# Kernel tuning notes

Hardware: AMD Instinct MI355X
Metric: run time of the kernel (lower is better)

Reference implementation:

```python
import jax, jax.numpy as jnp
import numpy as np

TEMPERATURE = 8.0  # sqrt(d_k=64)
NEG = -1e15


def setup_inputs() -> dict:
    key = jax.random.key(0)
    k1, k2, k3, k4, k5 = jax.random.split(key, 5)
    BH, L, D = 64, 1024, 64  # B=4 examples x H=16 heads
    B = 4
    q = jax.random.normal(k1, (BH, L, D), dtype=jnp.float32)
    k = jax.random.normal(k2, (BH, L, D), dtype=jnp.float32)
    v = jax.random.normal(k3, (BH, L, D), dtype=jnp.float32)
    mask = jax.random.randint(k4, (BH, L, L), 0, 2).astype(jnp.bool_)
    edge = jax.random.randint(k5, (B, L, L), 0, 2).astype(jnp.int32)
    return {"q": q, "k": k, "v": v, "mask": mask, "edge": edge}


def reference(q, k, v, mask, edge):
    # attn = q @ k^T / temperature : [BH, L, L]
    attn = jnp.einsum('bld,bmd->blm', q, k) / TEMPERATURE
    # edge.repeat(BH // B, 1, 1): torch repeat == tile along batch dim
    rep = attn.shape[0] // edge.shape[0]
    edge_t = jnp.tile(edge, (rep, 1, 1))
    attn = jnp.where(edge_t == 0, NEG, attn)
    attn = jnp.where(mask, NEG, attn)
    attn = jax.nn.softmax(attn, axis=2)
    # dropout p=0 -> identity
    output = jnp.einsum('blm,bmd->bld', attn, v)
    return (output, attn)
```

## Files before the change

### kernel.cpp

```cpp
#include <hip/hip_runtime.h>
#include <hip/hip_bf16.h>

#define L_ 1024
#define BH_ 64
#define NEGV (-1e15f)
#define QSCALE 0.18033688011112043f

typedef float f32x4 __attribute__((ext_vector_type(4)));
typedef short s16x8 __attribute__((ext_vector_type(8)));
typedef unsigned short ushort_t;

__device__ __forceinline__ unsigned short f2bf(float f) {
    return __builtin_bit_cast(unsigned short, __float2bfloat16(f));
}
__device__ __forceinline__ unsigned selw(uint4 v, int i) {
    switch (i) { case 0: return v.x; case 1: return v.y; case 2: return v.z; default: return v.w; }
}
__device__ __forceinline__ unsigned spread4(unsigned n) {
    return (n & 1u) | ((n & 2u) << 3) | ((n & 4u) << 6) | ((n & 8u) << 9);
}
__device__ __forceinline__ unsigned pack_bytes_nz(uint4 m) {
    unsigned u = 0;
    #pragma unroll
    for (int k = 0; k < 4; ++k) {
        const unsigned x = selw(m, k);
        u |= ((x & 0x000000FFu) ? 1u : 0u) << (k * 4 + 0);
        u |= ((x & 0x0000FF00u) ? 1u : 0u) << (k * 4 + 1);
        u |= ((x & 0x00FF0000u) ? 1u : 0u) << (k * 4 + 2);
        u |= ((x & 0xFF000000u) ? 1u : 0u) << (k * 4 + 3);
    }
    return u;
}
__device__ __forceinline__ void gl_lds16(const void* g, void* l) {
    __builtin_amdgcn_global_load_lds(
        (const __attribute__((address_space(1))) unsigned int*)g,
        (__attribute__((address_space(3))) unsigned int*)l, 16, 0, 0);
}

template<bool TESTZERO>
__device__ __forceinline__ unsigned row_bits_i32(uint4 e0, uint4 e1, uint4 e2, uint4 e3, int ln)
{
    #define BAL_(v) (TESTZERO ? __ballot((v) == 0u) : __ballot((v) != 0u))
    const unsigned long long b00 = BAL_(e0.x), b01 = BAL_(e0.y), b02 = BAL_(e0.z), b03 = BAL_(e0.w);
    const unsigned long long b10 = BAL_(e1.x), b11 = BAL_(e1.y), b12 = BAL_(e1.z), b13 = BAL_(e1.w);
    const unsigned long long b20 = BAL_(e2.x), b21 = BAL_(e2.y), b22 = BAL_(e2.z), b23 = BAL_(e2.w);
    const unsigned long long b30 = BAL_(e3.x), b31 = BAL_(e3.y), b32 = BAL_(e3.z), b33 = BAL_(e3.w);
    #undef BAL_
    const int q0 = ln >> 4, sh = (ln & 15) << 2;
    unsigned u = 0;
    unsigned long long bp;
    bp = q0 == 0 ? b00 : q0 == 1 ? b10 : q0 == 2 ? b20 : b30;
    u |= spread4((unsigned)((bp >> sh) & 0xF)) << 0;
    bp = q0 == 0 ? b01 : q0 == 1 ? b11 : q0 == 2 ? b21 : b31;
    u |= spread4((unsigned)((bp >> sh) & 0xF)) << 1;
    bp = q0 == 0 ? b02 : q0 == 1 ? b12 : q0 == 2 ? b22 : b32;
    u |= spread4((unsigned)((bp >> sh) & 0xF)) << 2;
    bp = q0 == 0 ? b03 : q0 == 1 ? b13 : q0 == 2 ? b23 : b33;
    u |= spread4((unsigned)((bp >> sh) & 0xF)) << 3;
    return u;
}

__global__ __launch_bounds__(256)
void prep(const float* __restrict__ qp, const float* __restrict__ kp,
          const float* __restrict__ vp, const unsigned char* __restrict__ maskp,
          const int* __restrict__ edgep, ushort_t* __restrict__ ws)
{
    __shared__ float tile[128][68];
    ushort_t* Kp = ws;
    ushort_t* Vp = ws + (1u << 22);
    ushort_t* Qp = ws + (2u << 22);
    ushort_t* Mp = ws + (3u << 22);

    const int b = blockIdx.x;
    const int t = threadIdx.x;

    if (b < 1024) {
        const int wv = t >> 6, ln = t & 63;
        const int rid = (b << 2) + wv;
        const int eb = rid >> 10, row = rid & 1023;

        unsigned det = 0;
        const unsigned* mu = (const unsigned*)maskp;
        #pragma unroll
        for (int i = 0; i < 16; ++i) det |= mu[i];
        const bool mask_i32 = ((det & 0xFFFFFF00u) == 0u);

        unsigned ewv;
        {
            const int rb = ((eb << 10) + row) << 10;
            const uint4 e0 = *((const uint4*)(edgep + rb) + ln);
            const uint4 e1 = *((const uint4*)(edgep + rb + 256) + ln);
            const uint4 e2 = *((const uint4*)(edgep + rb + 512) + ln);
            const uint4 e3 = *((const uint4*)(edgep + rb + 768) + ln);
            ewv = row_bits_i32<true>(e0, e1, e2, e3, ln);
        }
        const int pp = ((ln & 7) << 3) + (ln >> 3);
        for (int bq = 0; bq < 16; ++bq) {
            const int bh = (bq << 2) + eb;
            unsigned u = ewv;
            if (!mask_i32) {
                const uint4 m = *((const uint4*)(maskp + ((size_t)((bh << 10) + row) << 10)) + ln);
                u |= pack_bytes_nz(m);
            } else {
                const int* mp = (const int*)maskp + ((size_t)((bh << 10) + row) << 10);
                const uint4 m0 = *((const uint4*)mp + ln);
                const uint4 m1 = *((const uint4*)(mp + 256) + ln);
                const uint4 m2 = *((const uint4*)(mp + 512) + ln);
                const uint4 m3 = *((const uint4*)(mp + 768) + ln);
                u |= row_bits_i32<false>(m0, m1, m2, m3, ln);
            }
            Mp[((size_t)((bh << 10) + row) << 6) + pp] = (ushort_t)u;
        }
    } else if (b < 1536) {
        const int idx = b - 1024;
        const int bh = idx >> 3, vt = idx & 7;
        const float* vsrc = vp + (((size_t)(bh << 10) + (vt << 7)) << 6);
        #pragma unroll
        for (int i = 0; i < 8; ++i) {
            const int f4 = (i << 8) + t;
            const int k = f4 >> 4, d4 = f4 & 15;
            *(float4*)&tile[k][d4 << 2] = *((const float4*)vsrc + f4);
        }
        __syncthreads();
        ushort_t* dst = Vp + ((size_t)((bh << 3) + vt) << 13);
        #pragma unroll
        for (int i = 0; i < 4; ++i) {
            const int ci = (t << 2) + i;
            const int d = ci >> 4, p = ci & 15;
            const int c = p ^ (d & 7);
            s16x8 o;
            #pragma unroll
            for (int j = 0; j < 8; ++j) o[j] = (short)f2bf(tile[(c << 3) + j][d]);
            *(s16x8*)(dst + (ci << 3)) = o;
        }
    } else if (b < 2048) {
        const int idx = b - 1536;
        const int bh = idx >> 3, kt = idx & 7;
        const int r = t >> 1, h = t & 1;
        const float* src = kp + (((size_t)((bh << 10) + (kt << 7) + r)) << 6) + (h << 5);
        float v[32];
        #pragma unroll
        for (int j = 0; j < 8; ++j) *(float4*)&v[j << 2] = *((const float4*)src + j);
        ushort_t* dst = Kp + ((size_t)((bh << 3) + kt) << 13) + (r << 6);
        #pragma unroll
        for (int q = 0; q < 4; ++q) {
            const int c = (h << 2) + q;
            const int s = c ^ (r & 7);
            s16x8 o;
            #pragma unroll
            for (int j = 0; j < 8; ++j) o[j] = (short)f2bf(v[(q << 3) + j]);
            *(s16x8*)(dst + (s << 3)) = o;
        }
    } else {
        const int bh = b - 2048;
        const int wv = t >> 6, ln = t & 63;
        for (int i = 0; i < 16; ++i) {
            const int rt = (i << 2) + wv;
            const int r = (rt << 4) + (ln & 15), gq = ln >> 4;
            const float* src = qp + (((size_t)((bh << 10) + r)) << 6) + (gq << 3);
            const float4 q0 = *(const float4*)src;
            const float4 q1 = *(const float4*)(src + 4);
            const float4 q2 = *(const float4*)(src + 32);
            const float4 q3 = *(const float4*)(src + 36);
            s16x8 a, bfr;
            a[0]=(short)f2bf(q0.x*QSCALE); a[1]=(short)f2bf(q0.y*QSCALE);
            a[2]=(short)f2bf(q0.z*QSCALE); a[3]=(short)f2bf(q0.w*QSCALE);
            a[4]=(short)f2bf(q1.x*QSCALE); a[5]=(short)f2bf(q1.y*QSCALE);
            a[6]=(short)f2bf(q1.z*QSCALE); a[7]=(short)f2bf(q1.w*QSCALE);
            bfr[0]=(short)f2bf(q2.x*QSCALE); bfr[1]=(short)f2bf(q2.y*QSCALE);
            bfr[2]=(short)f2bf(q2.z*QSCALE); bfr[3]=(short)f2bf(q2.w*QSCALE);
            bfr[4]=(short)f2bf(q3.x*QSCALE); bfr[5]=(short)f2bf(q3.y*QSCALE);
            bfr[6]=(short)f2bf(q3.z*QSCALE); bfr[7]=(short)f2bf(q3.w*QSCALE);
            ushort_t* dst = Qp + ((size_t)((bh << 6) + rt) << 10) + (ln << 4);
            *(s16x8*)(dst) = a;
            *(s16x8*)(dst + 8) = bfr;
        }
    }
}

__global__ __launch_bounds__(512, 4)
void attn_main(const ushort_t* __restrict__ ws, float* __restrict__ outO,
               float* __restrict__ outA)
{
    __shared__ __align__(16) ushort_t p_lds[16 * 1024];
    __shared__ __align__(16) ushort_t stage[2][8192];
    __shared__ float part[16][8];
    __shared__ float gred[16];

    const ushort_t* Kp = ws;
    const ushort_t* Vp = ws + (1u << 22);
    const ushort_t* Qp = ws + (2u << 22);
    const ushort_t* Mp = ws + (3u << 22);

    const int tid = threadIdx.x, lane = tid & 63, w = tid >> 6;
    const int g = lane >> 4, ln = lane & 15;
    const int bid = blockIdx.x, xcd = bid & 7, slot = bid >> 3;
    const int bh = xcd + ((slot >> 6) << 3);
    const int rt = slot & 63;
    const int r0 = rt << 4;
    const int sb = w << 1;

    const ushort_t* qs = Qp + ((size_t)((bh << 6) + rt) << 10) + (lane << 4);
    const s16x8 a0 = *(const s16x8*)(qs);
    const s16x8 a1 = *(const s16x8*)(qs + 8);

    uint4 br[4];
    {
        const ushort_t* mrow = Mp + ((size_t)((bh << 10) + r0 + (g << 2)) << 6) + (w << 3);
        br[0] = *(const uint4*)(mrow);
        br[1] = *(const uint4*)(mrow + 64);
        br[2] = *(const uint4*)(mrow + 128);
        br[3] = *(const uint4*)(mrow + 192);
    }

    #define STAGE_(base, tt, cc)                                                   \
        gl_lds16(base + ((size_t)(bh) << 16) + ((tt) << 13) + ((sb + 0) << 9) + (lane << 3), \
                 &stage[cc][(sb + 0) << 9]);                                       \
        gl_lds16(base + ((size_t)(bh) << 16) + ((tt) << 13) + ((sb + 1) << 9) + (lane << 3), \
                 &stage[cc][(sb + 1) << 9]);

    STAGE_(Kp, 0, 0);
    __syncthreads();

    float rs[4] = {0.f, 0.f, 0.f, 0.f};

    #pragma unroll
    for (int kt = 0; kt < 8; ++kt) {
        const int cur = kt & 1, nxt = cur ^ 1;
        if (kt < 7) { STAGE_(Kp, kt + 1, nxt); }
        else        { STAGE_(Vp, 0, nxt); }

        const int rw = (w << 4) + ln;
        const char* kb = (const char*)stage[cur] + (rw << 7);
        const s16x8 b0 = *(const s16x8*)(kb + (((g)     ^ (rw & 7)) << 4));
        const s16x8 b1 = *(const s16x8*)(kb + (((4 + g) ^ (rw & 7)) << 4));
        f32x4 acc = {0.f, 0.f, 0.f, 0.f};
        acc = __builtin_amdgcn_mfma_f32_16x16x32_bf16(a0, b0, acc, 0, 0, 0);
        acc = __builtin_amdgcn_mfma_f32_16x16x32_bf16(a1, b1, acc, 0, 0, 0);

        #pragma unroll
        for (int reg = 0; reg < 4; ++reg) {
            float sv = acc[reg];
            const unsigned mw = selw(br[reg], kt >> 1);
            if ((mw >> (((kt & 1) << 4) + ln)) & 1u) sv = NEGV;
            const float e = __builtin_amdgcn_exp2f(sv);
            rs[reg] += e;
            const int prow = (g << 2) + reg;
            char* pd = (char*)p_lds + (prow << 11)
                     + ((((kt << 4) + (w << 1) + (ln >> 3)) ^ (prow & 7)) << 4)
                     + ((ln & 7) << 1);
            *(ushort_t*)pd = f2bf(e);
        }
        __syncthreads();
    }

    #pragma unroll
    for (int reg = 0; reg < 4; ++reg) {
        float s = rs[reg];
        s += __shfl_xor(s, 1);
        s += __shfl_xor(s, 2);
        s += __shfl_xor(s, 4);
        s += __shfl_xor(s, 8);
        if (ln == 0) part[(g << 2) + reg][w] = s;
    }
    __syncthreads();
    if (tid < 16) {
        float s = part[tid][0];
        #pragma unroll
        for (int i = 1; i < 8; ++i) s += part[tid][i];
        gred[tid] = __builtin_amdgcn_rcpf(s);
    }
    __syncthreads();

    const int dt = w & 3, kh = w >> 2;
    f32x4 acco = {0.f, 0.f, 0.f, 0.f};
    #pragma unroll
    for (int ut = 0; ut < 8; ++ut) {
        const int cur = ut & 1, nxt = cur ^ 1;
        if (ut < 7) { STAGE_(Vp, ut + 1, nxt); }

        const char* pl = (const char*)p_lds + (ln << 11);
        const s16x8 pa0 = *(const s16x8*)(pl + ((((ut << 4) + (kh << 3) + g)     ^ (ln & 7)) << 4));
        const s16x8 pa1 = *(const s16x8*)(pl + ((((ut << 4) + (kh << 3) + 4 + g) ^ (ln & 7)) << 4));
        const char* vb = (const char*)stage[cur] + (((dt << 4) + ln) << 8);
        const s16x8 vb0 = *(const s16x8*)(vb + ((((kh << 3) + g)     ^ (ln & 7)) << 4));
        const s16x8 vb1 = *(const s16x8*)(vb + ((((kh << 3) + 4 + g) ^ (ln & 7)) << 4));
        acco = __builtin_amdgcn_mfma_f32_16x16x32_bf16(pa0, vb0, acco, 0, 0, 0);
        acco = __builtin_amdgcn_mfma_f32_16x16x32_bf16(pa1, vb1, acco, 0, 0, 0);
        __syncthreads();
    }
    #undef STAGE_

    float* op = (float*)&stage[0][0];
    if (kh == 1) {
        #pragma unroll
        for (int reg = 0; reg < 4; ++reg)
            op[((dt << 4) + (g << 2) + reg) * 17 + ln] = acco[reg];
    }
    __syncthreads();
    if (kh == 0) {
        #pragma unroll
        for (int reg = 0; reg < 4; ++reg) {
            const int rl = (g << 2) + reg;
            outO[((size_t)((bh << 10) + r0 + rl) << 6) + (dt << 4) + ln] =
                (acco[reg] + op[((dt << 4) + rl) * 17 + ln]) * gred[rl];
        }
    }

    {
        const char* src = (const char*)p_lds;
        float* dstf = outA + ((size_t)((bh << 10) + r0) << 10);
        #pragma unroll
        for (int i = 0; i < 4; ++i) {
            const unsigned boff = (unsigned)((i * 512 + tid) << 4);
            const int rl = (int)(boff >> 11);
            const float rinv = gred[rl];
            const uint4 d4 = *(const uint4*)(src + (boff ^ ((rl & 7) << 4)));
            float4 f0, f1;
            f0.x = __builtin_bit_cast(float, d4.x << 16) * rinv;
            f0.y = __builtin_bit_cast(float, d4.x & 0xFFFF0000u) * rinv;
            f0.z = __builtin_bit_cast(float, d4.y << 16) * rinv;
            f0.w = __builtin_bit_cast(float, d4.y & 0xFFFF0000u) * rinv;
            f1.x = __builtin_bit_cast(float, d4.z << 16) * rinv;
            f1.y = __builtin_bit_cast(float, d4.z & 0xFFFF0000u) * rinv;
            f1.z = __builtin_bit_cast(float, d4.w << 16) * rinv;
            f1.w = __builtin_bit_cast(float, d4.w & 0xFFFF0000u) * rinv;
            char* db = (char*)dstf + ((size_t)boff << 1);
            *(float4*)db = f0;
            *(float4*)(db + 16) = f1;
        }
    }
}

__global__ __launch_bounds__(512)
void attn_fb(const float* __restrict__ qp, const float* __restrict__ kp,
             const float* __restrict__ vp, const unsigned char* __restrict__ maskp,
             const int* __restrict__ edgep, float* __restrict__ outO,
             float* __restrict__ outA)
{
    __shared__ __align__(16) ushort_t p_lds[16 * 1024];
    __shared__ float part[16][8];
    __shared__ float gred[16];
    __shared__ float opart[4][16][17];

    const int tid = threadIdx.x, lane = tid & 63, w = tid >> 6;
    const int g = lane >> 4, ln = lane & 15;
    const int bid = blockIdx.x, xcd = bid & 7, slot = bid >> 3;
    const int bh = xcd + ((slot >> 6) << 3);
    const int r0 = (slot & 63) << 4;
    const int c0 = w << 7;

    unsigned det = 0;
    const unsigned* mu = (const unsigned*)maskp;
    #pragma unroll
    for (int i = 0; i < 16; ++i) det |= mu[i];
    const bool mask_i32 = ((det & 0xFFFFFF00u) == 0u);

    const float* qb = qp + (((size_t)((bh << 10) + r0 + ln)) << 6) + (g << 3);
    s16x8 a0, a1;
    #pragma unroll
    for (int j = 0; j < 8; ++j) {
        a0[j] = (short)f2bf(qb[j] * QSCALE);
        a1[j] = (short)f2bf(qb[j + 32] * QSCALE);
    }

    f32x4 acc[8];
    #pragma unroll
    for (int nt = 0; nt < 8; ++nt) acc[nt] = (f32x4){0.f, 0.f, 0.f, 0.f};
    #pragma unroll
    for (int nt = 0; nt < 8; ++nt) {
        const float* kb = kp + (((size_t)((bh << 10) + c0 + (nt << 4) + ln)) << 6) + (g << 3);
        s16x8 b0, b1;
        #pragma unroll
        for (int j = 0; j < 8; ++j) {
            b0[j] = (short)f2bf(kb[j]);
            b1[j] = (short)f2bf(kb[j + 32]);
        }
        acc[nt] = __builtin_amdgcn_mfma_f32_16x16x32_bf16(a0, b0, acc[nt], 0, 0, 0);
        acc[nt] = __builtin_amdgcn_mfma_f32_16x16x32_bf16(a1, b1, acc[nt], 0, 0, 0);
    }

    float rs[4] = {0.f, 0.f, 0.f, 0.f};
    #pragma unroll
    for (int reg = 0; reg < 4; ++reg) {
        const int row = r0 + (g << 2) + reg;
        #pragma unroll
        for (int nt = 0; nt < 8; ++nt) {
            const int col = c0 + (nt << 4) + ln;
            float sv = acc[nt][reg];
            int mv;
            if (mask_i32) mv = ((const int*)maskp)[((size_t)((bh << 10) + row) << 10) + col];
            else          mv = (int)maskp[((size_t)((bh << 10) + row) << 10) + col];
            if (edgep[((size_t)((((bh & 3) << 10) + row)) << 10) + col] == 0 || mv != 0) sv = NEGV;
            const float e = __builtin_amdgcn_exp2f(sv);
            rs[reg] += e;
            const int rl = (g << 2) + reg;
            const unsigned off = ((unsigned)((rl << 11) | (col << 1))) ^ ((rl & 7) << 4);
            *(ushort_t*)((char*)p_lds + off) = f2bf(e);
        }
    }
    #pragma unroll
    for (int reg = 0; reg < 4; ++reg) {
        float s = rs[reg];
        s += __shfl_xor(s, 1);
        s += __shfl_xor(s, 2);
        s += __shfl_xor(s, 4);
        s += __shfl_xor(s, 8);
        if (ln == 0) part[(g << 2) + reg][w] = s;
    }
    __syncthreads();
    if (tid < 16) {
        float s = part[tid][0];
        #pragma unroll
        for (int i = 1; i < 8; ++i) s += part[tid][i];
        gred[tid] = __builtin_amdgcn_rcpf(s);
    }
    __syncthreads();

    const int dt = w & 3, kh = w >> 2;
    f32x4 acco = {0.f, 0.f, 0.f, 0.f};
    for (int kt = 0; kt < 16; ++kt) {
        const int ktg = (kh << 4) + kt;
        const unsigned offA = ((unsigned)((ln << 11) | (ktg << 6) | (g << 4))) ^ ((ln & 7) << 4);
        const s16x8 pa = *(const s16x8*)((const char*)p_lds + offA);
        s16x8 vb;
        #pragma unroll
        for (int j = 0; j < 8; ++j)
            vb[j] = (short)f2bf(vp[((size_t)((bh << 10) + (ktg << 5) + (g << 3) + j) << 6) + (dt << 4) + ln]);
        acco = __builtin_amdgcn_mfma_f32_16x16x32_bf16(pa, vb, acco, 0, 0, 0);
    }
    if (kh == 1) {
        #pragma unroll
        for (int reg = 0; reg < 4; ++reg)
            opart[dt][(g << 2) + reg][ln] = acco[reg];
    }
    __syncthreads();
    if (kh == 0) {
        #pragma unroll
        for (int reg = 0; reg < 4; ++reg) {
            const int rl = (g << 2) + reg;
            outO[((size_t)((bh << 10) + r0 + rl) << 6) + (dt << 4) + ln] =
                (acco[reg] + opart[dt][rl][ln]) * gred[rl];
        }
    }
    {
        const char* src = (const char*)p_lds;
        float* dstf = outA + ((size_t)((bh << 10) + r0) << 10);
        #pragma unroll
        for (int i = 0; i < 4; ++i) {
            const unsigned boff = (unsigned)((i * 512 + tid) << 4);
            const int rl = (int)(boff >> 11);
            const float rinv = gred[rl];
            const uint4 d4 = *(const uint4*)(src + (boff ^ ((rl & 7) << 4)));
            float4 f0, f1;
            f0.x = __builtin_bit_cast(float, d4.x << 16) * rinv;
            f0.y = __builtin_bit_cast(float, d4.x & 0xFFFF0000u) * rinv;
            f0.z = __builtin_bit_cast(float, d4.y << 16) * rinv;
            f0.w = __builtin_bit_cast(float, d4.y & 0xFFFF0000u) * rinv;
            f1.x = __builtin_bit_cast(float, d4.z << 16) * rinv;
            f1.y = __builtin_bit_cast(float, d4.z & 0xFFFF0000u) * rinv;
            f1.z = __builtin_bit_cast(float, d4.w << 16) * rinv;
            f1.w = __builtin_bit_cast(float, d4.w & 0xFFFF0000u) * rinv;
            char* db = (char*)dstf + ((size_t)boff << 1);
            *(float4*)db = f0;
            *(float4*)(db + 16) = f1;
        }
    }
}

extern "C" void kernel_launch(void* const* d_in, const int* in_sizes, int n_in,
                              void* d_out, int out_size, void* d_ws, size_t ws_size,
                              hipStream_t stream)
{
    (void)in_sizes; (void)n_in; (void)out_size;
    const float* qp = (const float*)d_in[0];
    const float* kp = (const float*)d_in[1];
    const float* vp = (const float*)d_in[2];
    const unsigned char* maskp = (const unsigned char*)d_in[3];
    const int* edgep = (const int*)d_in[4];

    float* outO = (float*)d_out;
    float* outA = outO + ((long long)BH_ * L_ * 64);

    const size_t need = (size_t)32 * 1024 * 1024;
    if (d_ws != nullptr && ws_size >= need) {
        ushort_t* ws = (ushort_t*)d_ws;
        prep<<<2112, 256, 0, stream>>>(qp, kp, vp, maskp, edgep, ws);
        attn_main<<<4096, 512, 0, stream>>>(ws, outO, outA);
    } else {
        attn_fb<<<4096, 512, 0, stream>>>(qp, kp, vp, maskp, edgep, outO, outA);
    }
}
```

Baseline: 239.5 us.

## Read mask directly in main kernel and drop LDS staging of K/V

```diff
diff --git a/kernel.cpp b/kernel.cpp
--- a/kernel.cpp
+++ b/kernel.cpp
@@ -18,23 +18,6 @@
 }
 __device__ __forceinline__ unsigned spread4(unsigned n) {
     return (n & 1u) | ((n & 2u) << 3) | ((n & 4u) << 6) | ((n & 8u) << 9);
-}
-__device__ __forceinline__ unsigned pack_bytes_nz(uint4 m) {
-    unsigned u = 0;
-    #pragma unroll
-    for (int k = 0; k < 4; ++k) {
-        const unsigned x = selw(m, k);
-        u |= ((x & 0x000000FFu) ? 1u : 0u) << (k * 4 + 0);
-        u |= ((x & 0x0000FF00u) ? 1u : 0u) << (k * 4 + 1);
-        u |= ((x & 0x00FF0000u) ? 1u : 0u) << (k * 4 + 2);
-        u |= ((x & 0xFF000000u) ? 1u : 0u) << (k * 4 + 3);
-    }
-    return u;
-}
-__device__ __forceinline__ void gl_lds16(const void* g, void* l) {
-    __builtin_amdgcn_global_load_lds(
-        (const __attribute__((address_space(1))) unsigned int*)g,
-        (__attribute__((address_space(3))) unsigned int*)l, 16, 0, 0);
 }
 
 template<bool TESTZERO>
@@ -62,57 +45,37 @@
 
 __global__ __launch_bounds__(256)
 void prep(const float* __restrict__ qp, const float* __restrict__ kp,
-          const float* __restrict__ vp, const unsigned char* __restrict__ maskp,
-          const int* __restrict__ edgep, ushort_t* __restrict__ ws)
+          const float* __restrict__ vp, const int* __restrict__ edgep,
+          ushort_t* __restrict__ ws)
 {
     __shared__ float tile[128][68];
     ushort_t* Kp = ws;
     ushort_t* Vp = ws + (1u << 22);
     ushort_t* Qp = ws + (2u << 22);
-    ushort_t* Mp = ws + (3u << 22);
+    ushort_t* Ep = ws + (3u << 22);
 
     const int b = blockIdx.x;
     const int t = threadIdx.x;
 
-    if (b < 1024) {
-        const int wv = t >> 6, ln = t & 63;
-        const int rid = (b << 2) + wv;
-        const int eb = rid >> 10, row = rid & 1023;
-
-        unsigned det = 0;
-        const unsigned* mu = (const unsigned*)maskp;
-        #pragma unroll
-        for (int i = 0; i < 16; ++i) det |= mu[i];
-        const bool mask_i32 = ((det & 0xFFFFFF00u) == 0u);
-
-        unsigned ewv;
-        {
-            const int rb = ((eb << 10) + row) << 10;
-            const uint4 e0 = *((const uint4*)(edgep + rb) + ln);
-            const uint4 e1 = *((const uint4*)(edgep + rb + 256) + ln);
-            const uint4 e2 = *((const uint4*)(edgep + rb + 512) + ln);
-            const uint4 e3 = *((const uint4*)(edgep + rb + 768) + ln);
-            ewv = row_bits_i32<true>(e0, e1, e2, e3, ln);
-        }
-        const int pp = ((ln & 7) << 3) + (ln >> 3);
-        for (int bq = 0; bq < 16; ++bq) {
-            const int bh = (bq << 2) + eb;
-            unsigned u = ewv;
-            if (!mask_i32) {
-                const uint4 m = *((const uint4*)(maskp + ((size_t)((bh << 10) + row) << 10)) + ln);
-                u |= pack_bytes_nz(m);
-            } else {
-                const int* mp = (const int*)maskp + ((size_t)((bh << 10) + row) << 10);
-                const uint4 m0 = *((const uint4*)mp + ln);
-                const uint4 m1 = *((const uint4*)(mp + 256) + ln);
-                const uint4 m2 = *((const uint4*)(mp + 512) + ln);
-                const uint4 m3 = *((const uint4*)(mp + 768) + ln);
-                u |= row_bits_i32<false>(m0, m1, m2, m3, ln);
-            }
-            Mp[((size_t)((bh << 10) + row) << 6) + pp] = (ushort_t)u;
-        }
-    } else if (b < 1536) {
-        const int idx = b - 1024;
+    if (b < 512) {
+        const int bh = b >> 3, kt = b & 7;
+        const int r = t >> 1, h = t & 1;
+        const float* src = kp + (((size_t)((bh << 10) + (kt << 7) + r)) << 6) + (h << 5);
+        float v[32];
+        #pragma unroll
+        for (int j = 0; j < 8; ++j) *(float4*)&v[j << 2] = *((const float4*)src + j);
+        ushort_t* dst = Kp + ((size_t)((bh << 3) + kt) << 13) + (r << 6);
+        #pragma unroll
+        for (int q = 0; q < 4; ++q) {
+            const int c = (h << 2) + q;
+            const int s = c ^ (r & 7);
+            s16x8 o;
+            #pragma unroll
+            for (int j = 0; j < 8; ++j) o[j] = (short)f2bf(v[(q << 3) + j]);
+            *(s16x8*)(dst + (s << 3)) = o;
+        }
+    } else if (b < 1024) {
+        const int idx = b - 512;
         const int bh = idx >> 3, vt = idx & 7;
         const float* vsrc = vp + (((size_t)(bh << 10) + (vt << 7)) << 6);
         #pragma unroll
@@ -133,26 +96,8 @@
             for (int j = 0; j < 8; ++j) o[j] = (short)f2bf(tile[(c << 3) + j][d]);
             *(s16x8*)(dst + (ci << 3)) = o;
         }
-    } else if (b < 2048) {
-        const int idx = b - 1536;
-        const int bh = idx >> 3, kt = idx & 7;
-        const int r = t >> 1, h = t & 1;
-        const float* src = kp + (((size_t)((bh << 10) + (kt << 7) + r)) << 6) + (h << 5);
-        float v[32];
-        #pragma unroll
-        for (int j = 0; j < 8; ++j) *(float4*)&v[j << 2] = *((const float4*)src + j);
-        ushort_t* dst = Kp + ((size_t)((bh << 3) + kt) << 13) + (r << 6);
-        #pragma unroll
-        for (int q = 0; q < 4; ++q) {
-            const int c = (h << 2) + q;
-            const int s = c ^ (r & 7);
-            s16x8 o;
-            #pragma unroll
-            for (int j = 0; j < 8; ++j) o[j] = (short)f2bf(v[(q << 3) + j]);
-            *(s16x8*)(dst + (s << 3)) = o;
-        }
-    } else {
-        const int bh = b - 2048;
+    } else if (b < 1088) {
+        const int bh = b - 1024;
         const int wv = t >> 6, ln = t & 63;
         for (int i = 0; i < 16; ++i) {
             const int rt = (i << 2) + wv;
@@ -175,22 +120,38 @@
             *(s16x8*)(dst) = a;
             *(s16x8*)(dst + 8) = bfr;
         }
-    }
-}
-
-__global__ __launch_bounds__(512, 4)
-void attn_main(const ushort_t* __restrict__ ws, float* __restrict__ outO,
-               float* __restrict__ outA)
+    } else {
+        const int b2 = b - 1088;
+        const int wv = t >> 6, ln = t & 63;
+        #pragma unroll 4
+        for (int it = 0; it < 16; ++it) {
+            const int rid = (b2 << 6) + (it << 2) + wv;
+            const int eb = rid >> 10, row = rid & 1023;
+            const int rb = ((eb << 10) + row) << 10;
+            const uint4 e0 = *((const uint4*)(edgep + rb) + ln);
+            const uint4 e1 = *((const uint4*)(edgep + rb + 256) + ln);
+            const uint4 e2 = *((const uint4*)(edgep + rb + 512) + ln);
+            const uint4 e3 = *((const uint4*)(edgep + rb + 768) + ln);
+            const unsigned u = row_bits_i32<true>(e0, e1, e2, e3, ln);
+            const int pp = ((ln & 7) << 3) + (ln >> 3);
+            Ep[((size_t)rid << 6) + pp] = (ushort_t)u;
+        }
+    }
+}
+
+__global__ __launch_bounds__(512, 6)
+void attn_main(const unsigned char* __restrict__ maskp, const ushort_t* __restrict__ ws,
+               float* __restrict__ outO, float* __restrict__ outA)
 {
     __shared__ __align__(16) ushort_t p_lds[16 * 1024];
-    __shared__ __align__(16) ushort_t stage[2][8192];
     __shared__ float part[16][8];
     __shared__ float gred[16];
+    __shared__ float opart[4][16][17];
 
     const ushort_t* Kp = ws;
     const ushort_t* Vp = ws + (1u << 22);
     const ushort_t* Qp = ws + (2u << 22);
-    const ushort_t* Mp = ws + (3u << 22);
+    const ushort_t* Ep = ws + (3u << 22);
 
     const int tid = threadIdx.x, lane = tid & 63, w = tid >> 6;
     const int g = lane >> 4, ln = lane & 15;
@@ -198,51 +159,59 @@
     const int bh = xcd + ((slot >> 6) << 3);
     const int rt = slot & 63;
     const int r0 = rt << 4;
-    const int sb = w << 1;
+
+    unsigned det = 0;
+    const unsigned* mu = (const unsigned*)maskp;
+    #pragma unroll
+    for (int i = 0; i < 16; ++i) det |= mu[i];
+    const bool mask_i32 = ((det & 0xFFFFFF00u) == 0u);
 
     const ushort_t* qs = Qp + ((size_t)((bh << 6) + rt) << 10) + (lane << 4);
     const s16x8 a0 = *(const s16x8*)(qs);
     const s16x8 a1 = *(const s16x8*)(qs + 8);
 
     uint4 br[4];
-    {
-        const ushort_t* mrow = Mp + ((size_t)((bh << 10) + r0 + (g << 2)) << 6) + (w << 3);
-        br[0] = *(const uint4*)(mrow);
-        br[1] = *(const uint4*)(mrow + 64);
-        br[2] = *(const uint4*)(mrow + 128);
-        br[3] = *(const uint4*)(mrow + 192);
-    }
-
-    #define STAGE_(base, tt, cc)                                                   \
-        gl_lds16(base + ((size_t)(bh) << 16) + ((tt) << 13) + ((sb + 0) << 9) + (lane << 3), \
-                 &stage[cc][(sb + 0) << 9]);                                       \
-        gl_lds16(base + ((size_t)(bh) << 16) + ((tt) << 13) + ((sb + 1) << 9) + (lane << 3), \
-                 &stage[cc][(sb + 1) << 9]);
-
-    STAGE_(Kp, 0, 0);
-    __syncthreads();
-
+    #pragma unroll
+    for (int reg = 0; reg < 4; ++reg)
+        br[reg] = *(const uint4*)(Ep + ((size_t)((((bh & 3) << 10) + r0 + (g << 2) + reg)) << 6) + (w << 3));
+
+    const size_t mrow = ((size_t)((bh << 10) + r0 + (g << 2)) << 10);
     float rs[4] = {0.f, 0.f, 0.f, 0.f};
 
     #pragma unroll
     for (int kt = 0; kt < 8; ++kt) {
-        const int cur = kt & 1, nxt = cur ^ 1;
-        if (kt < 7) { STAGE_(Kp, kt + 1, nxt); }
-        else        { STAGE_(Vp, 0, nxt); }
+        uint4 mq[4];
+        if (!mask_i32) {
+            #pragma unroll
+            for (int reg = 0; reg < 4; ++reg)
+                mq[reg] = *(const uint4*)(maskp + mrow + ((size_t)reg << 10) + (kt << 7) + (w << 4));
+        } else {
+            #pragma unroll
+            for (int reg = 0; reg < 4; ++reg)
+                mq[reg] = *(const uint4*)((const int*)maskp + mrow + ((size_t)reg << 10) + (kt << 7) + (w << 4) + (ln & 12));
+        }
 
         const int rw = (w << 4) + ln;
-        const char* kb = (const char*)stage[cur] + (rw << 7);
-        const s16x8 b0 = *(const s16x8*)(kb + (((g)     ^ (rw & 7)) << 4));
-        const s16x8 b1 = *(const s16x8*)(kb + (((4 + g) ^ (rw & 7)) << 4));
+        const ushort_t* kb = Kp + ((size_t)bh << 16) + (kt << 13) + (rw << 6);
+        const s16x8 b0 = *(const s16x8*)(kb + ((g ^ (rw & 7)) << 3));
+        const s16x8 b1 = *(const s16x8*)(kb + (((4 + g) ^ (rw & 7)) << 3));
+
         f32x4 acc = {0.f, 0.f, 0.f, 0.f};
         acc = __builtin_amdgcn_mfma_f32_16x16x32_bf16(a0, b0, acc, 0, 0, 0);
         acc = __builtin_amdgcn_mfma_f32_16x16x32_bf16(a1, b1, acc, 0, 0, 0);
 
         #pragma unroll
         for (int reg = 0; reg < 4; ++reg) {
+            bool msk;
+            if (!mask_i32) {
+                msk = ((selw(mq[reg], ln >> 2) >> ((ln & 3) << 3)) & 0xFFu) != 0u;
+            } else {
+                msk = selw(mq[reg], ln & 3) != 0u;
+            }
+            const unsigned ew = selw(br[reg], kt >> 1);
+            msk = msk || (((ew >> (((kt & 1) << 4) + ln)) & 1u) != 0u);
             float sv = acc[reg];
-            const unsigned mw = selw(br[reg], kt >> 1);
-            if ((mw >> (((kt & 1) << 4) + ln)) & 1u) sv = NEGV;
+            if (msk) sv = NEGV;
             const float e = __builtin_amdgcn_exp2f(sv);
             rs[reg] += e;
             const int prow = (g << 2) + reg;
@@ -251,7 +220,6 @@
                      + ((ln & 7) << 1);
             *(ushort_t*)pd = f2bf(e);
         }
-        __syncthreads();
     }
 
     #pragma unroll
@@ -274,28 +242,23 @@
 
     const int dt = w & 3, kh = w >> 2;
     f32x4 acco = {0.f, 0.f, 0.f, 0.f};
+    const ushort_t* vrow = Vp + ((size_t)bh << 16) + (((dt << 4) + ln) << 7);
+    const int vsw = ln & 7;
     #pragma unroll
     for (int ut = 0; ut < 8; ++ut) {
-        const int cur = ut & 1, nxt = cur ^ 1;
-        if (ut < 7) { STAGE_(Vp, ut + 1, nxt); }
-
+        const s16x8 vb0 = *(const s16x8*)(vrow + (ut << 13) + ((((kh << 3) + g)     ^ vsw) << 3));
+        const s16x8 vb1 = *(const s16x8*)(vrow + (ut << 13) + ((((kh << 3) + 4 + g) ^ vsw) << 3));
         const char* pl = (const char*)p_lds + (ln << 11);
-        const s16x8 pa0 = *(const s16x8*)(pl + ((((ut << 4) + (kh << 3) + g)     ^ (ln & 7)) << 4));
-        const s16x8 pa1 = *(const s16x8*)(pl + ((((ut << 4) + (kh << 3) + 4 + g) ^ (ln & 7)) << 4));
-        const char* vb = (const char*)stage[cur] + (((dt << 4) + ln) << 8);
-        const s16x8 vb0 = *(const s16x8*)(vb + ((((kh << 3) + g)     ^ (ln & 7)) << 4));
-        const s16x8 vb1 = *(const s16x8*)(vb + ((((kh << 3) + 4 + g) ^ (ln & 7)) << 4));
+        const s16x8 pa0 = *(const s16x8*)(pl + ((((ut << 4) + (kh << 3) + g)     ^ vsw) << 4));
+        const s16x8 pa1 = *(const s16x8*)(pl + ((((ut << 4) + (kh << 3) + 4 + g) ^ vsw) << 4));
         acco = __builtin_amdgcn_mfma_f32_16x16x32_bf16(pa0, vb0, acco, 0, 0, 0);
         acco = __builtin_amdgcn_mfma_f32_16x16x32_bf16(pa1, vb1, acco, 0, 0, 0);
-        __syncthreads();
-    }
-    #undef STAGE_
-
-    float* op = (float*)&stage[0][0];
+    }
+
     if (kh == 1) {
         #pragma unroll
         for (int reg = 0; reg < 4; ++reg)
-            op[((dt << 4) + (g << 2) + reg) * 17 + ln] = acco[reg];
+            opart[dt][(g << 2) + reg][ln] = acco[reg];
     }
     __syncthreads();
     if (kh == 0) {
@@ -303,7 +266,7 @@
         for (int reg = 0; reg < 4; ++reg) {
             const int rl = (g << 2) + reg;
             outO[((size_t)((bh << 10) + r0 + rl) << 6) + (dt << 4) + ln] =
-                (acco[reg] + op[((dt << 4) + rl) * 17 + ln]) * gred[rl];
+                (acco[reg] + opart[dt][rl][ln]) * gred[rl];
         }
     }
 
@@ -485,8 +448,8 @@
     const size_t need = (size_t)32 * 1024 * 1024;
     if (d_ws != nullptr && ws_size >= need) {
         ushort_t* ws = (ushort_t*)d_ws;
-        prep<<<2112, 256, 0, stream>>>(qp, kp, vp, maskp, edgep, ws);
-        attn_main<<<4096, 512, 0, stream>>>(ws, outO, outA);
+        prep<<<1152, 256, 0, stream>>>(qp, kp, vp, edgep, ws);
+        attn_main<<<4096, 512, 0, stream>>>(maskp, ws, outO, outA);
     } else {
         attn_fb<<<4096, 512, 0, stream>>>(qp, kp, vp, maskp, edgep, outO, outA);
     }
```

Result: slower. 277.5 us (+15.9%).

## Load K/V fragments directly into registers instead of LDS staging

Applied to the files above, without the earlier changes.

```diff
diff --git a/kernel.cpp b/kernel.cpp
--- a/kernel.cpp
+++ b/kernel.cpp
@@ -30,11 +30,6 @@
         u |= ((x & 0xFF000000u) ? 1u : 0u) << (k * 4 + 3);
     }
     return u;
-}
-__device__ __forceinline__ void gl_lds16(const void* g, void* l) {
-    __builtin_amdgcn_global_load_lds(
-        (const __attribute__((address_space(1))) unsigned int*)g,
-        (__attribute__((address_space(3))) unsigned int*)l, 16, 0, 0);
 }
 
 template<bool TESTZERO>
@@ -74,45 +69,25 @@
     const int b = blockIdx.x;
     const int t = threadIdx.x;
 
-    if (b < 1024) {
-        const int wv = t >> 6, ln = t & 63;
-        const int rid = (b << 2) + wv;
-        const int eb = rid >> 10, row = rid & 1023;
-
-        unsigned det = 0;
-        const unsigned* mu = (const unsigned*)maskp;
-        #pragma unroll
-        for (int i = 0; i < 16; ++i) det |= mu[i];
-        const bool mask_i32 = ((det & 0xFFFFFF00u) == 0u);
-
-        unsigned ewv;
-        {
-            const int rb = ((eb << 10) + row) << 10;
-            const uint4 e0 = *((const uint4*)(edgep + rb) + ln);
-            const uint4 e1 = *((const uint4*)(edgep + rb + 256) + ln);
-            const uint4 e2 = *((const uint4*)(edgep + rb + 512) + ln);
-            const uint4 e3 = *((const uint4*)(edgep + rb + 768) + ln);
-            ewv = row_bits_i32<true>(e0, e1, e2, e3, ln);
-        }
-        const int pp = ((ln & 7) << 3) + (ln >> 3);
-        for (int bq = 0; bq < 16; ++bq) {
-            const int bh = (bq << 2) + eb;
-            unsigned u = ewv;
-            if (!mask_i32) {
-                const uint4 m = *((const uint4*)(maskp + ((size_t)((bh << 10) + row) << 10)) + ln);
-                u |= pack_bytes_nz(m);
-            } else {
-                const int* mp = (const int*)maskp + ((size_t)((bh << 10) + row) << 10);
-                const uint4 m0 = *((const uint4*)mp + ln);
-                const uint4 m1 = *((const uint4*)(mp + 256) + ln);
-                const uint4 m2 = *((const uint4*)(mp + 512) + ln);
-                const uint4 m3 = *((const uint4*)(mp + 768) + ln);
-                u |= row_bits_i32<false>(m0, m1, m2, m3, ln);
-            }
-            Mp[((size_t)((bh << 10) + row) << 6) + pp] = (ushort_t)u;
-        }
-    } else if (b < 1536) {
-        const int idx = b - 1024;
+    if (b < 512) {
+        const int bh = b >> 3, kt = b & 7;
+        const int r = t >> 1, h = t & 1;
+        const float* src = kp + (((size_t)((bh << 10) + (kt << 7) + r)) << 6) + (h << 5);
+        float v[32];
+        #pragma unroll
+        for (int j = 0; j < 8; ++j) *(float4*)&v[j << 2] = *((const float4*)src + j);
+        ushort_t* dst = Kp + ((size_t)((bh << 3) + kt) << 13) + (r << 6);
+        #pragma unroll
+        for (int q = 0; q < 4; ++q) {
+            const int c = (h << 2) + q;
+            const int s = c ^ (r & 7);
+            s16x8 o;
+            #pragma unroll
+            for (int j = 0; j < 8; ++j) o[j] = (short)f2bf(v[(q << 3) + j]);
+            *(s16x8*)(dst + (s << 3)) = o;
+        }
+    } else if (b < 1024) {
+        const int idx = b - 512;
         const int bh = idx >> 3, vt = idx & 7;
         const float* vsrc = vp + (((size_t)(bh << 10) + (vt << 7)) << 6);
         #pragma unroll
@@ -133,26 +108,8 @@
             for (int j = 0; j < 8; ++j) o[j] = (short)f2bf(tile[(c << 3) + j][d]);
             *(s16x8*)(dst + (ci << 3)) = o;
         }
-    } else if (b < 2048) {
-        const int idx = b - 1536;
-        const int bh = idx >> 3, kt = idx & 7;
-        const int r = t >> 1, h = t & 1;
-        const float* src = kp + (((size_t)((bh << 10) + (kt << 7) + r)) << 6) + (h << 5);
-        float v[32];
-        #pragma unroll
-        for (int j = 0; j < 8; ++j) *(float4*)&v[j << 2] = *((const float4*)src + j);
-        ushort_t* dst = Kp + ((size_t)((bh << 3) + kt) << 13) + (r << 6);
-        #pragma unroll
-        for (int q = 0; q < 4; ++q) {
-            const int c = (h << 2) + q;
-            const int s = c ^ (r & 7);
-            s16x8 o;
-            #pragma unroll
-            for (int j = 0; j < 8; ++j) o[j] = (short)f2bf(v[(q << 3) + j]);
-            *(s16x8*)(dst + (s << 3)) = o;
-        }
-    } else {
-        const int bh = b - 2048;
+    } else if (b < 1088) {
+        const int bh = b - 1024;
         const int wv = t >> 6, ln = t & 63;
         for (int i = 0; i < 16; ++i) {
             const int rt = (i << 2) + wv;
@@ -175,17 +132,54 @@
             *(s16x8*)(dst) = a;
             *(s16x8*)(dst + 8) = bfr;
         }
-    }
-}
-
-__global__ __launch_bounds__(512, 4)
+    } else {
+        const int wv = t >> 6, ln = t & 63;
+        const int rid = ((b - 1088) << 2) + wv;
+        const int eb = rid >> 10, row = rid & 1023;
+
+        unsigned det = 0;
+        const unsigned* mu = (const unsigned*)maskp;
+        #pragma unroll
+        for (int i = 0; i < 16; ++i) det |= mu[i];
+        const bool mask_i32 = ((det & 0xFFFFFF00u) == 0u);
+
+        unsigned ewv;
+        {
+            const int rb = ((eb << 10) + row) << 10;
+            const uint4 e0 = *((const uint4*)(edgep + rb) + ln);
+            const uint4 e1 = *((const uint4*)(edgep + rb + 256) + ln);
+            const uint4 e2 = *((const uint4*)(edgep + rb + 512) + ln);
+            const uint4 e3 = *((const uint4*)(edgep + rb + 768) + ln);
+            ewv = row_bits_i32<true>(e0, e1, e2, e3, ln);
+        }
+        const int pp = ((ln & 7) << 3) + (ln >> 3);
+        for (int bq = 0; bq < 16; ++bq) {
+            const int bh = (bq << 2) + eb;
+            unsigned u = ewv;
+            if (!mask_i32) {
+                const uint4 m = *((const uint4*)(maskp + ((size_t)((bh << 10) + row) << 10)) + ln);
+                u |= pack_bytes_nz(m);
+            } else {
+                const int* mp = (const int*)maskp + ((size_t)((bh << 10) + row) << 10);
+                const uint4 m0 = *((const uint4*)mp + ln);
+                const uint4 m1 = *((const uint4*)(mp + 256) + ln);
+                const uint4 m2 = *((const uint4*)(mp + 512) + ln);
+                const uint4 m3 = *((const uint4*)(mp + 768) + ln);
+                u |= row_bits_i32<false>(m0, m1, m2, m3, ln);
+            }
+            Mp[((size_t)((bh << 10) + row) << 6) + pp] = (ushort_t)u;
+        }
+    }
+}
+
+__global__ __launch_bounds__(512, 5)
 void attn_main(const ushort_t* __restrict__ ws, float* __restrict__ outO,
                float* __restrict__ outA)
 {
     __shared__ __align__(16) ushort_t p_lds[16 * 1024];
-    __shared__ __align__(16) ushort_t stage[2][8192];
     __shared__ float part[16][8];
     __shared__ float gred[16];
+    __shared__ float opart[4][16][17];
 
     const ushort_t* Kp = ws;
     const ushort_t* Vp = ws + (1u << 22);
@@ -198,51 +192,52 @@
     const int bh = xcd + ((slot >> 6) << 3);
     const int rt = slot & 63;
     const int r0 = rt << 4;
-    const int sb = w << 1;
+    const int rw = (w << 4) + ln;
+    const int ksw = rw & 7, vsw = ln & 7;
+    const int dt = w & 3, kh = w >> 2;
 
     const ushort_t* qs = Qp + ((size_t)((bh << 6) + rt) << 10) + (lane << 4);
     const s16x8 a0 = *(const s16x8*)(qs);
     const s16x8 a1 = *(const s16x8*)(qs + 8);
 
     uint4 br[4];
-    {
-        const ushort_t* mrow = Mp + ((size_t)((bh << 10) + r0 + (g << 2)) << 6) + (w << 3);
-        br[0] = *(const uint4*)(mrow);
-        br[1] = *(const uint4*)(mrow + 64);
-        br[2] = *(const uint4*)(mrow + 128);
-        br[3] = *(const uint4*)(mrow + 192);
-    }
-
-    #define STAGE_(base, tt, cc)                                                   \
-        gl_lds16(base + ((size_t)(bh) << 16) + ((tt) << 13) + ((sb + 0) << 9) + (lane << 3), \
-                 &stage[cc][(sb + 0) << 9]);                                       \
-        gl_lds16(base + ((size_t)(bh) << 16) + ((tt) << 13) + ((sb + 1) << 9) + (lane << 3), \
-                 &stage[cc][(sb + 1) << 9]);
-
-    STAGE_(Kp, 0, 0);
-    __syncthreads();
+    #pragma unroll
+    for (int reg = 0; reg < 4; ++reg)
+        br[reg] = *(const uint4*)(Mp + ((size_t)((bh << 10) + r0 + (g << 2) + reg) << 6) + (w << 3));
+
+    const ushort_t* kbase = Kp + ((size_t)bh << 16) + (rw << 6);
+    const int ko0 = (g ^ ksw) << 3, ko1 = ((4 + g) ^ ksw) << 3;
+    const ushort_t* vrow = Vp + ((size_t)bh << 16) + (((dt << 4) + ln) << 7);
+    const int vo0 = (((kh << 3) + g) ^ vsw) << 3, vo1 = (((kh << 3) + 4 + g) ^ vsw) << 3;
+
+    s16x8 kb0[8], kb1[8], vb0[8], vb1[8];
+    kb0[0] = *(const s16x8*)(kbase + ko0);
+    kb1[0] = *(const s16x8*)(kbase + ko1);
+    kb0[1] = *(const s16x8*)(kbase + (1 << 13) + ko0);
+    kb1[1] = *(const s16x8*)(kbase + (1 << 13) + ko1);
 
     float rs[4] = {0.f, 0.f, 0.f, 0.f};
 
     #pragma unroll
     for (int kt = 0; kt < 8; ++kt) {
-        const int cur = kt & 1, nxt = cur ^ 1;
-        if (kt < 7) { STAGE_(Kp, kt + 1, nxt); }
-        else        { STAGE_(Vp, 0, nxt); }
-
-        const int rw = (w << 4) + ln;
-        const char* kb = (const char*)stage[cur] + (rw << 7);
-        const s16x8 b0 = *(const s16x8*)(kb + (((g)     ^ (rw & 7)) << 4));
-        const s16x8 b1 = *(const s16x8*)(kb + (((4 + g) ^ (rw & 7)) << 4));
+        if (kt < 6) {
+            kb0[kt + 2] = *(const s16x8*)(kbase + ((kt + 2) << 13) + ko0);
+            kb1[kt + 2] = *(const s16x8*)(kbase + ((kt + 2) << 13) + ko1);
+        } else {
+            const int ut = kt - 6;
+            vb0[ut] = *(const s16x8*)(vrow + (ut << 13) + vo0);
+            vb1[ut] = *(const s16x8*)(vrow + (ut << 13) + vo1);
+        }
+
         f32x4 acc = {0.f, 0.f, 0.f, 0.f};
-        acc = __builtin_amdgcn_mfma_f32_16x16x32_bf16(a0, b0, acc, 0, 0, 0);
-        acc = __builtin_amdgcn_mfma_f32_16x16x32_bf16(a1, b1, acc, 0, 0, 0);
+        acc = __builtin_amdgcn_mfma_f32_16x16x32_bf16(a0, kb0[kt], acc, 0, 0, 0);
+        acc = __builtin_amdgcn_mfma_f32_16x16x32_bf16(a1, kb1[kt], acc, 0, 0, 0);
 
         #pragma unroll
         for (int reg = 0; reg < 4; ++reg) {
+            const unsigned ew = selw(br[reg], kt >> 1);
             float sv = acc[reg];
-            const unsigned mw = selw(br[reg], kt >> 1);
-            if ((mw >> (((kt & 1) << 4) + ln)) & 1u) sv = NEGV;
+            if ((ew >> (((kt & 1) << 4) + ln)) & 1u) sv = NEGV;
             const float e = __builtin_amdgcn_exp2f(sv);
             rs[reg] += e;
             const int prow = (g << 2) + reg;
@@ -251,7 +246,6 @@
                      + ((ln & 7) << 1);
             *(ushort_t*)pd = f2bf(e);
         }
-        __syncthreads();
     }
 
     #pragma unroll
@@ -272,30 +266,24 @@
     }
     __syncthreads();
 
-    const int dt = w & 3, kh = w >> 2;
     f32x4 acco = {0.f, 0.f, 0.f, 0.f};
     #pragma unroll
     for (int ut = 0; ut < 8; ++ut) {
-        const int cur = ut & 1, nxt = cur ^ 1;
-        if (ut < 7) { STAGE_(Vp, ut + 1, nxt); }
-
+        if (ut < 6) {
+            vb0[ut + 2] = *(const s16x8*)(vrow + ((ut + 2) << 13) + vo0);
+            vb1[ut + 2] = *(const s16x8*)(vrow + ((ut + 2) << 13) + vo1);
+        }
         const char* pl = (const char*)p_lds + (ln << 11);
-        const s16x8 pa0 = *(const s16x8*)(pl + ((((ut << 4) + (kh << 3) + g)     ^ (ln & 7)) << 4));
-        const s16x8 pa1 = *(const s16x8*)(pl + ((((ut << 4) + (kh << 3) + 4 + g) ^ (ln & 7)) << 4));
-        const char* vb = (const char*)stage[cur] + (((dt << 4) + ln) << 8);
-        const s16x8 vb0 = *(const s16x8*)(vb + ((((kh << 3) + g)     ^ (ln & 7)) << 4));
-        const s16x8 vb1 = *(const s16x8*)(vb + ((((kh << 3) + 4 + g) ^ (ln & 7)) << 4));
-        acco = __builtin_amdgcn_mfma_f32_16x16x32_bf16(pa0, vb0, acco, 0, 0, 0);
-        acco = __builtin_amdgcn_mfma_f32_16x16x32_bf16(pa1, vb1, acco, 0, 0, 0);
-        __syncthreads();
-    }
-    #undef STAGE_
-
-    float* op = (float*)&stage[0][0];
+        const s16x8 pa0 = *(const s16x8*)(pl + ((((ut << 4) + (kh << 3) + g)     ^ vsw) << 4));
+        const s16x8 pa1 = *(const s16x8*)(pl + ((((ut << 4) + (kh << 3) + 4 + g) ^ vsw) << 4));
+        acco = __builtin_amdgcn_mfma_f32_16x16x32_bf16(pa0, vb0[ut], acco, 0, 0, 0);
+        acco = __builtin_amdgcn_mfma_f32_16x16x32_bf16(pa1, vb1[ut], acco, 0, 0, 0);
+    }
+
     if (kh == 1) {
         #pragma unroll
         for (int reg = 0; reg < 4; ++reg)
-            op[((dt << 4) + (g << 2) + reg) * 17 + ln] = acco[reg];
+            opart[dt][(g << 2) + reg][ln] = acco[reg];
     }
     __syncthreads();
     if (kh == 0) {
@@ -303,7 +291,7 @@
         for (int reg = 0; reg < 4; ++reg) {
             const int rl = (g << 2) + reg;
             outO[((size_t)((bh << 10) + r0 + rl) << 6) + (dt << 4) + ln] =
-                (acco[reg] + op[((dt << 4) + rl) * 17 + ln]) * gred[rl];
+                (acco[reg] + opart[dt][rl][ln]) * gred[rl];
         }
     }
 
```

Result: faster. 219.9 us (-8.2%).
